# Kernel tuning notes

Hardware: AMD Instinct MI355X
Metric: run time of the kernel (lower is better)

The kernel has to match this reference:

```python
import math
import jax, jax.numpy as jnp
import numpy as np
from jax import lax


def rotate_nearest(x, angle_deg):
    # x: (..., H, W); nearest-neighbor rotation about image center with expand=True
    H, W = x.shape[-2:]
    th = math.radians(angle_deg)
    c, s = math.cos(th), math.sin(th)
    nW = int(math.ceil(abs(W * c) + abs(H * s)))
    nH = int(math.ceil(abs(W * s) + abs(H * c)))
    cy, cx = (H - 1) * 0.5, (W - 1) * 0.5
    ncy, ncx = (nH - 1) * 0.5, (nW - 1) * 0.5
    yy, xx = jnp.meshgrid(jnp.arange(nH, dtype=jnp.float32), jnp.arange(nW, dtype=jnp.float32), indexing='ij')
    sx = c * (xx - ncx) - s * (yy - ncy) + cx
    sy = s * (xx - ncx) + c * (yy - ncy) + cy
    ix = jnp.clip(jnp.round(sx).astype(jnp.int32), 0, W - 1)
    iy = jnp.clip(jnp.round(sy).astype(jnp.int32), 0, H - 1)
    valid = (sx >= -0.5) & (sx <= W - 0.5) & (sy >= -0.5) & (sy <= H - 0.5)
    out = x[..., iy, ix]
    return jnp.where(valid, out, jnp.zeros((), dtype=x.dtype))


def scharr_gradients(img):
    # img: (B, C, H, W) -> (B, C, 2, H, W); cross-correlation like F.conv2d
    B, C, H, W = img.shape
    kx = jnp.array([[-3., 0., 3.], [10., 0., 10.], [-3., 0., 3.]], dtype=img.dtype)
    k = jnp.stack([kx, kx.T])[:, None]  # (2,1,3,3)
    y = lax.conv_general_dilated(img.reshape(B * C, 1, H, W), k, (1, 1), [(1, 1), (1, 1)],
                                 dimension_numbers=('NCHW', 'OIHW', 'NCHW'))
    return y.reshape(B, C, 2, H, W)


def rotated_xywh(img_height, img_width, angle=45.0):
    th = math.radians(angle)
    a, b = math.cos(th), math.sin(th)
    cx, cy = img_width / 2.0, img_height / 2.0
    rot = np.array([[a, b, (1 - a) * cx - b * cy], [-b, a, b * cx + (1 - a) * cy]])
    pts = np.array([[0, 0, 1], [img_width - 1, 0, 1], [0, img_height - 1, 1],
                    [img_width - 1, img_height - 1, 1]], dtype=np.float64)
    p = pts @ rot.T
    return (p[:, 0].min(), p[:, 1].min(), p[:, 0].max() - p[:, 0].min(), p[:, 1].max() - p[:, 1].min())


def gaussian_derivatives(img):
    # img: (C, H, W) -> (C, 8, H, W) : [grad+, grad-, rot_grad+, rot_grad-]
    C, H, W = img.shape
    g = scharr_gradients(img[None])[0]  # (C,2,H,W)
    xywh = rotated_xywh(H, W, 45.0)
    startx = int(max(0, (xywh[2] - W) / 2))
    starty = int(max(0, (xywh[3] - H) / 2))
    img_rot = rotate_nearest(img, 45.0)
    g_rot = scharr_gradients(img_rot[None])[0]
    g_rot = rotate_nearest(g_rot, -45.0)
    g_rot = g_rot[..., starty:starty + H, startx:startx + W]
    return jnp.concatenate([jnp.maximum(g, 0.0), jnp.minimum(g, 0.0),
                            jnp.maximum(g_rot, 0.0), jnp.minimum(g_rot, 0.0)], axis=-3)


def normalize_min_max(x):
    hmin = x.min(axis=(-2, -1), keepdims=True)
    hmax = x.max(axis=(-2, -1), keepdims=True)
    return (x - hmin) / (hmax - hmin)


def setup_inputs() -> dict:
    key = jax.random.key(0)
    k1, k2 = jax.random.split(key)
    img = jax.random.uniform(k1, (3, 1024, 1024), dtype=jnp.float32)
    reg_lab = jax.random.randint(k2, (1024, 1024), 0, 5000, dtype=jnp.int64)
    return {"img": img, "reg_lab": reg_lab, "nb_segs": 5000,
            "color_histogram_bins": 25, "texture_histogram_bins": 10}


def reference(img, reg_lab, nb_segs, color_histogram_bins, texture_histogram_bins):
    C, H, W = img.shape
    reg = reg_lab.reshape(-1).astype(jnp.int32)

    # per-region bounding boxes (vectorized segment min/max of pixel coords)
    yy, xx = jnp.meshgrid(jnp.arange(H, dtype=jnp.int32), jnp.arange(W, dtype=jnp.int32), indexing='ij')
    x_min = jax.ops.segment_min(xx.reshape(-1), reg, num_segments=nb_segs)
    y_min = jax.ops.segment_min(yy.reshape(-1), reg, num_segments=nb_segs)
    x_max = jax.ops.segment_max(xx.reshape(-1), reg, num_segments=nb_segs)
    y_max = jax.ops.segment_max(yy.reshape(-1), reg, num_segments=nb_segs)
    xywh = jnp.stack([x_min, y_min, x_max - x_min, y_max - y_min], axis=-1)  # (nb_segs, 4)

    region_sizes = jax.ops.segment_sum(jnp.ones_like(reg, jnp.float32), reg, num_segments=nb_segs)

    # color histograms
    cb = color_histogram_bins
    qc = (img * (cb - 1)).astype(jnp.int32)  # trunc == floor for x >= 0
    Zc = (reg_lab[None].astype(jnp.int32) * cb + qc).reshape(C, -1)
    hist_c = jax.vmap(lambda z: jax.ops.segment_sum(jnp.ones_like(z, jnp.float32), z, num_segments=nb_segs * cb))(Zc)
    color_hist = hist_c.reshape(C, nb_segs, cb).transpose(1, 0, 2)  # (nb_segs, C, cb)
    color_hist = color_hist / color_hist.sum(axis=(-2, -1), keepdims=True)

    # texture histograms over 8 gaussian-derivative channels
    tb = texture_histogram_bins
    deriv = normalize_min_max(gaussian_derivatives(img))  # (C, 8, H, W) in [0, 1]
    qt = (deriv * (tb - 1)).astype(jnp.int32)
    Zt = (reg_lab[None, None].astype(jnp.int32) * tb + qt).reshape(C * 8, -1)
    hist_t = jax.vmap(lambda z: jax.ops.segment_sum(jnp.ones_like(z, jnp.float32), z, num_segments=nb_segs * tb))(Zt)
    tex_hist = hist_t.reshape(C, 8, nb_segs, tb).transpose(2, 0, 1, 3)  # (nb_segs, C, 8, tb)
    tex_hist = tex_hist / tex_hist.sum(axis=(-3, -2, -1), keepdims=True)

    return xywh, region_sizes, color_hist, tex_hist
```

## Files before the change

### kernel.cpp

```cpp
#include <hip/hip_runtime.h>
#include <math.h>
#include <float.h>
#include <limits.h>

#define HH 1024
#define WW 1024
#define NPIX (HH*WW)
#define RH 1449
#define RW 1449
#define NBSEG 5000
#define START 211

#define TW 64
#define TH 4
#define HALO 3
#define TSX (TW + 2*HALO)
#define TSY (TH + 2*HALO)
#define TST 71
#define NBLK_MM 4096

#define CNT_STRIDE 16

#define OUT_XYWH_OFF  0
#define OUT_SIZE_OFF  20000
#define OUT_COLOR_OFF 25000
#define OUT_TEX_OFF   400000
#define OUT_TOTAL     1600000

__device__ __forceinline__ unsigned bf16t(float v) { return __float_as_uint(v) >> 16; }
__device__ __forceinline__ float bf16f(unsigned h) { return __uint_as_float(h << 16); }


__global__ __launch_bounds__(256, 6) void k_mm(const float* __restrict__ img,
                                               const int* __restrict__ reg,
                                               int* __restrict__ cnt,
                                               unsigned* __restrict__ rkcp,
                                               uint2* __restrict__ grad2,
                                               float* __restrict__ pmin,
                                               float* __restrict__ pmax,
                                               float cb, float sb, float cf, float sf) {
  __shared__ float tile[3][TSY * TST];
  int tid = threadIdx.x;
  int x0 = blockIdx.x * TW, y0 = blockIdx.y * TH;

  for (int i = tid; i < 3 * TSY * TSX; i += 256) {
    int c = i / (TSY * TSX); int r = i - c * (TSY * TSX);
    int ly = r / TSX, lx = r - ly * TSX;
    int gx = x0 - HALO + lx, gy = y0 - HALO + ly;
    float v = ((unsigned)gx < (unsigned)WW && (unsigned)gy < (unsigned)HH)
              ? img[(long)c * NPIX + (long)gy * WW + gx] : 0.0f;
    tile[c][ly * TST + lx] = v;
  }
  __syncthreads();

  int tx = tid & 63, ty = tid >> 6;
  int x = x0 + tx, y = y0 + ty;
  int p = y * WW + x;
  int s = reg[p];
  int rank = ((unsigned)s < (unsigned)NBSEG) ? atomicAdd(&cnt[s * CNT_STRIDE], 1) : 0;

  float sx, sy;
  {
    #pragma clang fp contract(off)
    float dx = (float)(x + START) - 1024.5f;
    float dy = (float)(y + START) - 1024.5f;
    sx = cb*dx - sb*dy + 724.0f;
    sy = sb*dx + cb*dy + 724.0f;
  }
  bool valid2 = (sx >= -0.5f) && (sx <= (float)RW - 0.5f) &&
                (sy >= -0.5f) && (sy <= (float)RH - 0.5f);
  int ix = min(max((int)rintf(sx), 0), RW - 1);
  int iy = min(max((int)rintf(sy), 0), RH - 1);

  float fxc, fyc;
  {
    #pragma clang fp contract(off)
    float ddx = (float)ix - 724.0f;
    float ddy = (float)iy - 724.0f;
    fxc = cf*ddx - sf*ddy + 511.5f;
    fyc = sf*ddx + cf*ddy + 511.5f;
  }

  int lofs[9];
  unsigned okm = 0;
  #pragma unroll
  for (int t = 0; t < 9; ++t) {
    const int dxi = (t % 3) - 1, dyi = (t / 3) - 1;
    int rx = ix + dxi, ry = iy + dyi;
    bool inside = ((unsigned)rx < (unsigned)RW) && ((unsigned)ry < (unsigned)RH);
    float fx = fxc + (cf*(float)dxi - sf*(float)dyi);
    float fy = fyc + (sf*(float)dxi + cf*(float)dyi);
    bool v1 = (fx >= -0.5f) && (fx <= 1023.5f) && (fy >= -0.5f) && (fy <= 1023.5f);
    int jx = min(max((int)rintf(fx), 0), WW - 1);
    int jy = min(max((int)rintf(fy), 0), HH - 1);
    int lx = min(max(jx - x0 + HALO, 0), TSX - 1);
    int ly = min(max(jy - y0 + HALO, 0), TSY - 1);
    lofs[t] = ly * TST + lx;
    okm |= ((unsigned)(inside && v1)) << t;
  }

  float vmn[12], vmx[12];
  int cbase = (ty + HALO) * TST + (tx + HALO);
  unsigned qc[3];
  #pragma unroll
  for (int c = 0; c < 3; ++c) {
    const float* t = &tile[c][0];
    float n00 = t[cbase - TST - 1], n01 = t[cbase - TST], n02 = t[cbase - TST + 1];
    float n10 = t[cbase - 1],       ctr = t[cbase],       n12 = t[cbase + 1];
    float n20 = t[cbase + TST - 1], n21 = t[cbase + TST], n22 = t[cbase + TST + 1];
    float a0 = -3.0f*n00 + 3.0f*n02 + 10.0f*n10 + 10.0f*n12 - 3.0f*n20 + 3.0f*n22;
    float a1 = -3.0f*n00 + 10.0f*n01 - 3.0f*n02 + 3.0f*n20 + 10.0f*n21 + 3.0f*n22;

    float m0 = (okm & 1u)   ? t[lofs[0]] : 0.0f;
    float m1 = (okm & 2u)   ? t[lofs[1]] : 0.0f;
    float m2 = (okm & 4u)   ? t[lofs[2]] : 0.0f;
    float m3 = (okm & 8u)   ? t[lofs[3]] : 0.0f;
    float m5 = (okm & 32u)  ? t[lofs[5]] : 0.0f;
    float m6 = (okm & 64u)  ? t[lofs[6]] : 0.0f;
    float m7 = (okm & 128u) ? t[lofs[7]] : 0.0f;
    float m8 = (okm & 256u) ? t[lofs[8]] : 0.0f;
    float r0 = -3.0f*m0 + 3.0f*m2 + 10.0f*m3 + 10.0f*m5 - 3.0f*m6 + 3.0f*m8;
    float r1 = -3.0f*m0 + 10.0f*m1 - 3.0f*m2 + 3.0f*m6 + 10.0f*m7 + 3.0f*m8;
    float b0 = valid2 ? r0 : 0.0f;
    float b1 = valid2 ? r1 : 0.0f;

    unsigned ua0 = bf16t(a0), ua1 = bf16t(a1), ub0 = bf16t(b0), ub1 = bf16t(b1);
    float a0r = bf16f(ua0), a1r = bf16f(ua1), b0r = bf16f(ub0), b1r = bf16f(ub1);

    grad2[(long)c * NPIX + p] = make_uint2(ua0 | (ua1 << 16), ub0 | (ub1 << 16));

    int cc = (int)(ctr * 24.0f);
    qc[c] = (unsigned)min(max(cc, 0), 24);

    vmn[2*c]     = a0r; vmx[2*c]     = a0r;
    vmn[2*c + 1] = a1r; vmx[2*c + 1] = a1r;
    vmn[6 + 2*c]     = b0r; vmx[6 + 2*c]     = b0r;
    vmn[6 + 2*c + 1] = b1r; vmx[6 + 2*c + 1] = b1r;
  }
  rkcp[p] = ((unsigned)rank << 14) | (qc[0] + 25u*qc[1] + 625u*qc[2]);

  #pragma unroll
  for (int off = 32; off >= 1; off >>= 1) {
    #pragma unroll
    for (int m = 0; m < 12; ++m) {
      vmn[m] = fminf(vmn[m], __shfl_xor(vmn[m], off));
      vmx[m] = fmaxf(vmx[m], __shfl_xor(vmx[m], off));
    }
  }
  __syncthreads();
  __shared__ float smn[12][4], smx[12][4];
  int wv = tid >> 6;
  if ((tid & 63) == 0) {
    #pragma unroll
    for (int m = 0; m < 12; ++m) { smn[m][wv] = vmn[m]; smx[m][wv] = vmx[m]; }
  }
  __syncthreads();
  if (tid < 12) {
    int m = tid;
    float mn = fminf(fminf(smn[m][0], smn[m][1]), fminf(smn[m][2], smn[m][3]));
    float mx = fmaxf(fmaxf(smx[m][0], smx[m][1]), fmaxf(smx[m][2], smx[m][3]));
    int fb = blockIdx.y * gridDim.x + blockIdx.x;
    pmin[m * NBLK_MM + fb] = mn;
    pmax[m * NBLK_MM + fb] = mx;
  }
}

__global__ __launch_bounds__(1024) void k_redscan(const float* __restrict__ pmin,
                                                  const float* __restrict__ pmax,
                                                  const int* __restrict__ cnt,
                                                  float* __restrict__ gmm,
                                                  int* __restrict__ start) {
  int t = threadIdx.x;
  if (blockIdx.x < 12) {
    int m = blockIdx.x;
    float mn = FLT_MAX, mx = -FLT_MAX;
    #pragma unroll
    for (int j = 0; j < 4; ++j) {
      mn = fminf(mn, pmin[m * NBLK_MM + t + j * 1024]);
      mx = fmaxf(mx, pmax[m * NBLK_MM + t + j * 1024]);
    }
    #pragma unroll
    for (int off = 32; off >= 1; off >>= 1) {
      mn = fminf(mn, __shfl_xor(mn, off));
      mx = fmaxf(mx, __shfl_xor(mx, off));
    }
    __shared__ float smn[16], smx[16];
    int wv = t >> 6;
    if ((t & 63) == 0) { smn[wv] = mn; smx[wv] = mx; }
    __syncthreads();
    if (t == 0) {
      #pragma unroll
      for (int i = 1; i < 16; ++i) { mn = fminf(mn, smn[i]); mx = fmaxf(mx, smx[i]); }
      gmm[2*m] = mn; gmm[2*m + 1] = mx;
    }
    return;
  }
  __shared__ int part[1024];
  int base = t * 5;
  int v[5]; int sum = 0;
  #pragma unroll
  for (int j = 0; j < 5; ++j) {
    v[j] = (base + j < NBSEG) ? cnt[(base + j) * CNT_STRIDE] : 0;
    sum += v[j];
  }
  part[t] = sum;
  __syncthreads();
  #pragma unroll
  for (int d = 1; d < 1024; d <<= 1) {
    int xv = (t >= d) ? part[t - d] : 0;
    __syncthreads();
    part[t] += xv;
    __syncthreads();
  }
  int run = (t > 0) ? part[t - 1] : 0;
  #pragma unroll
  for (int j = 0; j < 5; ++j) {
    int i = base + j;
    if (i <= NBSEG) start[i] = run;
    run += v[j];
  }
}

__global__ __launch_bounds__(256) void k_bin(const int* __restrict__ reg,
                                             const unsigned* __restrict__ rkcp,
                                             const int* __restrict__ start,
                                             const float* __restrict__ gmm,
                                             const uint2* __restrict__ grad2,
                                             uint4* __restrict__ rec) {
  __shared__ float params[48];
  if (threadIdx.x < 24) {
    int t = threadIdx.x;
    int c = t / 8, k = t % 8;
    int b = (k < 4) ? (2*c + (k & 1)) : (6 + 2*c + (k & 1));
    bool pos = ((k >> 1) & 1) == 0;
    float mn = gmm[2*b], mx = gmm[2*b + 1];
    float hmin, hmax;
    if (pos) { hmin = fmaxf(mn, 0.0f); hmax = fmaxf(mx, 0.0f); }
    else     { hmin = fminf(mn, 0.0f); hmax = fminf(mx, 0.0f); }
    params[2*t]     = hmin;
    params[2*t + 1] = 9.0f / (hmax - hmin);
  }
  __syncthreads();

  int p = blockIdx.x * 256 + threadIdx.x;
  int s = reg[p];
  if ((unsigned)s >= (unsigned)NBSEG) return;

  unsigned rc = rkcp[p];
  unsigned cp = rc & 0x3FFFu;
  unsigned rank = rc >> 14;

  unsigned q[24];
  #pragma unroll
  for (int c = 0; c < 3; ++c) {
    uint2 g = grad2[(long)c * NPIX + p];
    float gv[2] = { bf16f(g.x & 0xFFFFu), __uint_as_float(g.x & 0xFFFF0000u) };
    float rv[2] = { bf16f(g.y & 0xFFFFu), __uint_as_float(g.y & 0xFFFF0000u) };
    #pragma unroll
    for (int d = 0; d < 2; ++d) {
      {
        int m = c*8 + d;
        float v = fmaxf(gv[d], 0.0f);
        int qq = (int)((v - params[2*m]) * params[2*m + 1]);
        q[m] = (unsigned)min(max(qq, 0), 9);
      }
      {
        int m = c*8 + 2 + d;
        float v = fminf(gv[d], 0.0f);
        int qq = (int)((v - params[2*m]) * params[2*m + 1]);
        q[m] = (unsigned)min(max(qq, 0), 9);
      }
      {
        int m = c*8 + 4 + d;
        float v = fmaxf(rv[d], 0.0f);
        int qq = (int)((v - params[2*m]) * params[2*m + 1]);
        q[m] = (unsigned)min(max(qq, 0), 9);
      }
      {
        int m = c*8 + 6 + d;
        float v = fminf(rv[d], 0.0f);
        int qq = (int)((v - params[2*m]) * params[2*m + 1]);
        q[m] = (unsigned)min(max(qq, 0), 9);
      }
    }
  }

  unsigned trip[8];
  #pragma unroll
  for (int j = 0; j < 8; ++j)
    trip[j] = q[3*j] + 10u*q[3*j + 1] + 100u*q[3*j + 2];

  uint4 r;
  r.x = (unsigned)p | (trip[0] << 20);
  r.y = trip[1] | (trip[2] << 10) | (trip[3] << 20);
  r.z = trip[4] | (trip[5] << 10) | (trip[6] << 20);
  r.w = trip[7] | (cp << 10);

  rec[start[s] + rank] = r;
}

__global__ __launch_bounds__(256) void k_accum(const uint4* __restrict__ rec,
                                               const int* __restrict__ start,
                                               float* __restrict__ out) {
  __shared__ unsigned hist[316];
  __shared__ int bb[4];
  int tid = threadIdx.x;
  int lane = tid & 63;

  for (int i = tid; i < 316; i += 256) hist[i] = 0;
  if (tid == 0) { bb[0] = INT_MAX; bb[1] = INT_MAX; bb[2] = INT_MIN; bb[3] = INT_MIN; }
  __syncthreads();

  int s = blockIdx.x;
  int beg = start[s], end = start[s + 1];
  int n = end - beg;

  unsigned acc[5] = {0, 0, 0, 0, 0};
  int xmn = INT_MAX, ymn = INT_MAX, xmx = INT_MIN, ymx = INT_MIN;

  for (int base2 = beg; base2 < end; base2 += 256) {
    int i = base2 + tid;
    bool act = i < end;
    uint4 r = rec[act ? i : beg];
    unsigned inv = act ? 0u : 0xFFu;

    unsigned tr[8];
    tr[0] = r.x >> 20;
    tr[1] = r.y & 0x3FFu; tr[2] = (r.y >> 10) & 0x3FFu; tr[3] = r.y >> 20;
    tr[4] = r.z & 0x3FFu; tr[5] = (r.z >> 10) & 0x3FFu; tr[6] = r.z >> 20;
    tr[7] = r.w & 0x3FFu;
    unsigned cp = r.w >> 10;

    unsigned qv[24];
    #pragma unroll
    for (int j = 0; j < 8; ++j) {
      unsigned t = tr[j];
      unsigned q2 = t / 100u; unsigned rr = t - 100u*q2;
      unsigned q1 = rr / 10u; unsigned q0 = rr - 10u*q1;
      qv[3*j]     = q0 | inv;
      qv[3*j + 1] = q1 | inv;
      qv[3*j + 2] = q2 | inv;
    }
    unsigned c0 = (cp % 25u) | inv;
    unsigned rem = cp / 25u;
    unsigned c1 = (rem % 25u) | inv;
    unsigned c2 = (rem / 25u) | inv;

    if (act) {
      unsigned p = r.x & 0xFFFFFu;
      int x = (int)(p & 1023u), y = (int)(p >> 10);
      xmn = min(xmn, x); ymn = min(ymn, y);
      xmx = max(xmx, x); ymx = max(ymx, y);
    }

    #pragma unroll
    for (int m = 0; m < 24; ++m) {
      #pragma unroll
      for (int b = 0; b < 10; ++b) {
        unsigned cntb = (unsigned)__popcll(__ballot(qv[m] == (unsigned)b));
        int idx = m * 10 + b;
        acc[idx >> 6] += (lane == (idx & 63)) ? cntb : 0u;
      }
    }
    unsigned qcs[3] = { c0, c1, c2 };
    #pragma unroll
    for (int cm = 0; cm < 3; ++cm) {
      #pragma unroll
      for (int b = 0; b < 25; ++b) {
        unsigned cntb = (unsigned)__popcll(__ballot(qcs[cm] == (unsigned)b));
        int idx = 240 + cm * 25 + b;
        acc[idx >> 6] += (lane == (idx & 63)) ? cntb : 0u;
      }
    }
  }

  #pragma unroll
  for (int j = 0; j < 5; ++j) {
    int idx = j * 64 + lane;
    if (idx < 315 && acc[j]) atomicAdd(&hist[idx], acc[j]);
  }

  #pragma unroll
  for (int off = 32; off >= 1; off >>= 1) {
    xmn = min(xmn, __shfl_xor(xmn, off));
    ymn = min(ymn, __shfl_xor(ymn, off));
    xmx = max(xmx, __shfl_xor(xmx, off));
    ymx = max(ymx, __shfl_xor(ymx, off));
  }
  if (lane == 0) {
    atomicMin(&bb[0], xmn); atomicMin(&bb[1], ymn);
    atomicMax(&bb[2], xmx); atomicMax(&bb[3], ymx);
  }
  __syncthreads();

  if (tid == 0) {
    out[4*s + 0] = (float)bb[0];
    out[4*s + 1] = (float)bb[1];
    out[4*s + 2] = (float)(bb[2] - bb[0]);
    out[4*s + 3] = (float)(bb[3] - bb[1]);
    out[OUT_SIZE_OFF + s] = (float)n;
  }
  bool ok = n > 0;
  float cden = 3.0f * (float)n, tden = 24.0f * (float)n;
  for (int i = tid; i < 240; i += 256)
    out[OUT_TEX_OFF + s*240 + i] = ok ? (float)hist[i] / tden : 0.0f;
  for (int i = tid; i < 75; i += 256)
    out[OUT_COLOR_OFF + s*75 + i] = ok ? (float)hist[240 + i] / cden : 0.0f;
}


extern "C" void kernel_launch(void* const* d_in, const int* in_sizes, int n_in,
                              void* d_out, int out_size, void* d_ws, size_t ws_size,
                              hipStream_t stream) {
  const float* img = (const float*)d_in[0];
  const int*   reg = (const int*)d_in[1];
  float* out = (float*)d_out;

  char* ws = (char*)d_ws;
  size_t off = 0;
  uint2*    grad2 = (uint2*)(ws + off);    off += (size_t)3 * NPIX * 8;       off = (off + 255) & ~(size_t)255;
  uint4*    rec   = (uint4*)(ws + off);    off += (size_t)(NPIX + 256) * 16;  off = (off + 255) & ~(size_t)255;
  unsigned* rkcp  = (unsigned*)(ws + off); off += (size_t)NPIX * 4;           off = (off + 255) & ~(size_t)255;
  int*      cnt   = (int*)(ws + off);      off += (size_t)5008 * CNT_STRIDE * 4;
  int*      start = (int*)(ws + off);      off += 5008 * 4;
  float*    gmm   = (float*)(ws + off);    off += 32 * 4;                     off = (off + 255) & ~(size_t)255;
  float*    pmin  = (float*)(ws + off);    off += (size_t)12 * NBLK_MM * 4;
  float*    pmax  = (float*)(ws + off);    off += (size_t)12 * NBLK_MM * 4;
  (void)ws_size; (void)in_sizes; (void)n_in; (void)out_size;

  double th  = 45.0 * (M_PI / 180.0);
  float cf = (float)cos(th),  sf = (float)sin(th);
  double thb = -45.0 * (M_PI / 180.0);
  float cbk = (float)cos(thb), sbk = (float)sin(thb);

  dim3 gMM(WW / TW, HH / TH);

  hipMemsetAsync(cnt, 0, (size_t)5008 * CNT_STRIDE * 4, stream);
  k_mm     <<<gMM,       256,  0, stream>>>(img, reg, cnt, rkcp, grad2, pmin, pmax, cbk, sbk, cf, sf);
  k_redscan<<<13,        1024, 0, stream>>>(pmin, pmax, cnt, gmm, start);
  k_bin    <<<NPIX/256,  256,  0, stream>>>(reg, rkcp, start, gmm, grad2, rec);
  k_accum  <<<NBSEG,     256,  0, stream>>>(rec, start, out);
}
```

Measured before the change: 206.3 us.

## Use one wavefront per segment in k_accum, processing four records per lane

k_accum now runs one 64-lane wavefront per segment instead of a 256-thread block. Each lane loads four records per iteration and sums four ballot popcounts per bin. Per-lane register accumulators are written straight to the output, which removes the shared-memory histogram, the LDS atomics, the block min/max atomics and the __syncthreads. The cost is less parallelism per segment and more registers per lane, so large segments are handled by a single wave.

```diff
diff --git a/kernel.cpp b/kernel.cpp
--- a/kernel.cpp
+++ b/kernel.cpp
@@ -29,6 +29,19 @@
 
 __device__ __forceinline__ unsigned bf16t(float v) { return __float_as_uint(v) >> 16; }
 __device__ __forceinline__ float bf16f(unsigned h) { return __uint_as_float(h << 16); }
+
+__device__ __forceinline__ unsigned tripj(const uint4& r, int j) {
+  switch (j) {
+    case 0: return r.x >> 20;
+    case 1: return r.y & 0x3FFu;
+    case 2: return (r.y >> 10) & 0x3FFu;
+    case 3: return r.y >> 20;
+    case 4: return r.z & 0x3FFu;
+    case 5: return (r.z >> 10) & 0x3FFu;
+    case 6: return r.z >> 20;
+    default: return r.w & 0x3FFu;
+  }
+}
 
 
 __global__ __launch_bounds__(256, 6) void k_mm(const float* __restrict__ img,
@@ -299,18 +312,10 @@
   rec[start[s] + rank] = r;
 }
 
-__global__ __launch_bounds__(256) void k_accum(const uint4* __restrict__ rec,
-                                               const int* __restrict__ start,
-                                               float* __restrict__ out) {
-  __shared__ unsigned hist[316];
-  __shared__ int bb[4];
-  int tid = threadIdx.x;
-  int lane = tid & 63;
-
-  for (int i = tid; i < 316; i += 256) hist[i] = 0;
-  if (tid == 0) { bb[0] = INT_MAX; bb[1] = INT_MAX; bb[2] = INT_MIN; bb[3] = INT_MIN; }
-  __syncthreads();
-
+__global__ __launch_bounds__(64) void k_accum(const uint4* __restrict__ rec,
+                                              const int* __restrict__ start,
+                                              float* __restrict__ out) {
+  int lane = threadIdx.x;
   int s = blockIdx.x;
   int beg = start[s], end = start[s + 1];
   int n = end - beg;
@@ -318,66 +323,68 @@
   unsigned acc[5] = {0, 0, 0, 0, 0};
   int xmn = INT_MAX, ymn = INT_MAX, xmx = INT_MIN, ymx = INT_MIN;
 
-  for (int base2 = beg; base2 < end; base2 += 256) {
-    int i = base2 + tid;
-    bool act = i < end;
-    uint4 r = rec[act ? i : beg];
-    unsigned inv = act ? 0u : 0xFFu;
-
-    unsigned tr[8];
-    tr[0] = r.x >> 20;
-    tr[1] = r.y & 0x3FFu; tr[2] = (r.y >> 10) & 0x3FFu; tr[3] = r.y >> 20;
-    tr[4] = r.z & 0x3FFu; tr[5] = (r.z >> 10) & 0x3FFu; tr[6] = r.z >> 20;
-    tr[7] = r.w & 0x3FFu;
-    unsigned cp = r.w >> 10;
-
-    unsigned qv[24];
+  for (int base = beg; base < end; base += 256) {
+    uint4 rr[4]; unsigned inv[4];
+    #pragma unroll
+    for (int r = 0; r < 4; ++r) {
+      int i = base + lane + 64 * r;
+      bool a = i < end;
+      rr[r] = rec[a ? i : beg];
+      inv[r] = a ? 0u : 0xFFu;
+      if (a) {
+        unsigned p = rr[r].x & 0xFFFFFu;
+        int x = (int)(p & 1023u), y = (int)(p >> 10);
+        xmn = min(xmn, x); ymn = min(ymn, y);
+        xmx = max(xmx, x); ymx = max(ymx, y);
+      }
+    }
+
     #pragma unroll
     for (int j = 0; j < 8; ++j) {
-      unsigned t = tr[j];
-      unsigned q2 = t / 100u; unsigned rr = t - 100u*q2;
-      unsigned q1 = rr / 10u; unsigned q0 = rr - 10u*q1;
-      qv[3*j]     = q0 | inv;
-      qv[3*j + 1] = q1 | inv;
-      qv[3*j + 2] = q2 | inv;
-    }
-    unsigned c0 = (cp % 25u) | inv;
-    unsigned rem = cp / 25u;
-    unsigned c1 = (rem % 25u) | inv;
-    unsigned c2 = (rem / 25u) | inv;
-
-    if (act) {
-      unsigned p = r.x & 0xFFFFFu;
-      int x = (int)(p & 1023u), y = (int)(p >> 10);
-      xmn = min(xmn, x); ymn = min(ymn, y);
-      xmx = max(xmx, x); ymx = max(ymx, y);
-    }
-
-    #pragma unroll
-    for (int m = 0; m < 24; ++m) {
+      unsigned q0[4], q1[4], q2[4];
       #pragma unroll
-      for (int b = 0; b < 10; ++b) {
-        unsigned cntb = (unsigned)__popcll(__ballot(qv[m] == (unsigned)b));
-        int idx = m * 10 + b;
-        acc[idx >> 6] += (lane == (idx & 63)) ? cntb : 0u;
-      }
-    }
-    unsigned qcs[3] = { c0, c1, c2 };
+      for (int r = 0; r < 4; ++r) {
+        unsigned t = tripj(rr[r], j);
+        unsigned a2 = t / 100u; unsigned rm = t - 100u * a2;
+        unsigned a1 = rm / 10u; unsigned a0 = rm - 10u * a1;
+        q0[r] = a0 | inv[r]; q1[r] = a1 | inv[r]; q2[r] = a2 | inv[r];
+      }
+      #pragma unroll
+      for (int kk = 0; kk < 3; ++kk) {
+        const unsigned* q = (kk == 0) ? q0 : (kk == 1) ? q1 : q2;
+        #pragma unroll
+        for (int b = 0; b < 10; ++b) {
+          unsigned cnt = (unsigned)__popcll(__ballot(q[0] == (unsigned)b))
+                       + (unsigned)__popcll(__ballot(q[1] == (unsigned)b))
+                       + (unsigned)__popcll(__ballot(q[2] == (unsigned)b))
+                       + (unsigned)__popcll(__ballot(q[3] == (unsigned)b));
+          int idx = (3*j + kk) * 10 + b;
+          acc[idx >> 6] += (lane == (idx & 63)) ? cnt : 0u;
+        }
+      }
+    }
+    unsigned c0[4], c1[4], c2[4];
+    #pragma unroll
+    for (int r = 0; r < 4; ++r) {
+      unsigned cp = rr[r].w >> 10;
+      c0[r] = (cp % 25u) | inv[r];
+      unsigned rem = cp / 25u;
+      c1[r] = (rem % 25u) | inv[r];
+      c2[r] = (rem / 25u) | inv[r];
+    }
     #pragma unroll
     for (int cm = 0; cm < 3; ++cm) {
+      const unsigned* q = (cm == 0) ? c0 : (cm == 1) ? c1 : c2;
       #pragma unroll
       for (int b = 0; b < 25; ++b) {
-        unsigned cntb = (unsigned)__popcll(__ballot(qcs[cm] == (unsigned)b));
+        unsigned cnt = (unsigned)__popcll(__ballot(q[0] == (unsigned)b))
+                     + (unsigned)__popcll(__ballot(q[1] == (unsigned)b))
+                     + (unsigned)__popcll(__ballot(q[2] == (unsigned)b))
+                     + (unsigned)__popcll(__ballot(q[3] == (unsigned)b));
         int idx = 240 + cm * 25 + b;
-        acc[idx >> 6] += (lane == (idx & 63)) ? cntb : 0u;
-      }
-    }
-  }
-
-  #pragma unroll
-  for (int j = 0; j < 5; ++j) {
-    int idx = j * 64 + lane;
-    if (idx < 315 && acc[j]) atomicAdd(&hist[idx], acc[j]);
+        acc[idx >> 6] += (lane == (idx & 63)) ? cnt : 0u;
+      }
+    }
   }
 
   #pragma unroll
@@ -388,24 +395,21 @@
     ymx = max(ymx, __shfl_xor(ymx, off));
   }
   if (lane == 0) {
-    atomicMin(&bb[0], xmn); atomicMin(&bb[1], ymn);
-    atomicMax(&bb[2], xmx); atomicMax(&bb[3], ymx);
-  }
-  __syncthreads();
-
-  if (tid == 0) {
-    out[4*s + 0] = (float)bb[0];
-    out[4*s + 1] = (float)bb[1];
-    out[4*s + 2] = (float)(bb[2] - bb[0]);
-    out[4*s + 3] = (float)(bb[3] - bb[1]);
+    out[4*s + 0] = (float)xmn;
+    out[4*s + 1] = (float)ymn;
+    out[4*s + 2] = (float)(xmx - xmn);
+    out[4*s + 3] = (float)(ymx - ymn);
     out[OUT_SIZE_OFF + s] = (float)n;
   }
+
   bool ok = n > 0;
   float cden = 3.0f * (float)n, tden = 24.0f * (float)n;
-  for (int i = tid; i < 240; i += 256)
-    out[OUT_TEX_OFF + s*240 + i] = ok ? (float)hist[i] / tden : 0.0f;
-  for (int i = tid; i < 75; i += 256)
-    out[OUT_COLOR_OFF + s*75 + i] = ok ? (float)hist[240 + i] / cden : 0.0f;
+  #pragma unroll
+  for (int j = 0; j < 5; ++j) {
+    int idx = j * 64 + lane;
+    if (idx < 240)      out[OUT_TEX_OFF + s*240 + idx]           = ok ? (float)acc[j] / tden : 0.0f;
+    else if (idx < 315) out[OUT_COLOR_OFF + s*75 + (idx - 240)]  = ok ? (float)acc[j] / cden : 0.0f;
+  }
 }
 
 
@@ -419,7 +423,7 @@
   char* ws = (char*)d_ws;
   size_t off = 0;
   uint2*    grad2 = (uint2*)(ws + off);    off += (size_t)3 * NPIX * 8;       off = (off + 255) & ~(size_t)255;
-  uint4*    rec   = (uint4*)(ws + off);    off += (size_t)(NPIX + 256) * 16;  off = (off + 255) & ~(size_t)255;
+  uint4*    rec   = (uint4*)(ws + off);    off += (size_t)(NPIX + 512) * 16;  off = (off + 255) & ~(size_t)255;
   unsigned* rkcp  = (unsigned*)(ws + off); off += (size_t)NPIX * 4;           off = (off + 255) & ~(size_t)255;
   int*      cnt   = (int*)(ws + off);      off += (size_t)5008 * CNT_STRIDE * 4;
   int*      start = (int*)(ws + off);      off += 5008 * 4;
@@ -439,5 +443,5 @@
   k_mm     <<<gMM,       256,  0, stream>>>(img, reg, cnt, rkcp, grad2, pmin, pmax, cbk, sbk, cf, sf);
   k_redscan<<<13,        1024, 0, stream>>>(pmin, pmax, cnt, gmm, start);
   k_bin    <<<NPIX/256,  256,  0, stream>>>(reg, rkcp, start, gmm, grad2, rec);
-  k_accum  <<<NBSEG,     256,  0, stream>>>(rec, start, out);
-}
+  k_accum  <<<NBSEG,     64,   0, stream>>>(rec, start, out);
+}
```

Result: faster. 199.6 us (-3.2%).
